# Kernel optimization log

Measured on AMD Instinct MI355X. Metric: run time of the kernel, lower is better.

## Reference

```python
import jax, jax.numpy as jnp
import numpy as np

LMAX, MMAX = 4, 2
L1 = LMAX + 1                      # 5 coefficients with m=0
NL = [LMAX + 1 - m for m in range(MMAX + 1)]   # [5,4,3] degrees per |m|
K = (LMAX + 1) ** 2                # 25 full SH coefficients
KR = NL[0] + 2 * sum(NL[1:])       # 19 coefficients with |m|<=mmax
# degree l of each row in the reduced (m-primary) layout:
# m=0: l=0..4 | m=+1: l=1..4 | m=-1: l=1..4 | m=+2: l=2..4 | m=-2: l=2..4
L_IDX = np.array([0,1,2,3,4, 1,2,3,4, 1,2,3,4, 2,3,4, 2,3,4])


def so2_conv(x, rad, w0, b0, wr1, wi1, wr2, wi2, c_out, extra):
    """SO(2)-equivariant conv over m-primary layout x: [E, KR, c_in].
    rad: optional per-edge radial weights [E, sum_m nl_m*c_in]."""
    E, _, c_in = x.shape
    # m = 0 block
    x0 = x[:, :L1].reshape(E, L1 * c_in)
    if rad is not None:
        x0 = x0 * rad[:, :L1 * c_in]
    y0 = x0 @ w0 + b0
    out0 = y0[:, :L1 * c_out].reshape(E, L1, c_out)
    gating = y0[:, L1 * c_out:] if extra else None
    outs = [out0]
    off_x, off_r = L1, L1 * c_in
    for nl, wr, wi in ((NL[1], wr1, wi1), (NL[2], wr2, wi2)):
        xr = x[:, off_x:off_x + nl].reshape(E, nl * c_in)
        xi = x[:, off_x + nl:off_x + 2 * nl].reshape(E, nl * c_in)
        if rad is not None:
            rm = rad[:, off_r:off_r + nl * c_in]
            xr, xi = xr * rm, xi * rm
        yr = xr @ wr - xi @ wi   # complex-style SO2 mixing
        yi = xi @ wr + xr @ wi
        outs += [yr.reshape(E, nl, c_out), yi.reshape(E, nl, c_out)]
        off_x += 2 * nl
        off_r += nl * c_in
    return jnp.concatenate(outs, axis=1), gating


def gate_act(gating, x):
    """GateActivation: silu on l=0 scalars, sigmoid gates per degree l>=1."""
    E, _, H = x.shape
    g = jax.nn.sigmoid(gating).reshape(E, LMAX, H)
    g_ext = jnp.concatenate([jnp.ones((E, 1, H), x.dtype), g], axis=1)
    out = x * g_ext[:, L_IDX]           # l=0 row gated by 1, replaced below
    return out.at[:, 0].set(jax.nn.silu(x[:, 0]))


def setup_inputs() -> dict:
    key = jax.random.key(0)
    ks = jax.random.split(key, 32)
    E, N, C, H, D, RH = 50000, 2500, 64, 64, 128, 64
    c_in1 = 2 * C
    rad_dim = sum(nl * c_in1 for nl in NL)          # 1536
    extra = LMAX * H                                 # 256

    def w(k, shape):
        return jax.random.normal(k, shape, jnp.float32) / np.sqrt(shape[0])

    inp = {
        'node_feats': jax.random.normal(ks[0], (N, K, C), jnp.float32),
        'edge_embeds': jax.random.normal(ks[1], (E, D), jnp.float32),
        'wigner': jax.random.normal(ks[2], (E, KR, K), jnp.float32) / np.sqrt(K),
        'wigner_inv': jax.random.normal(ks[3], (E, K, KR), jnp.float32) / np.sqrt(KR),
        'edge_envelope': jax.random.uniform(ks[4], (E, 1, 1), jnp.float32),
        'rad_w1': w(ks[5], (D, RH)), 'rad_b1': jnp.zeros((RH,), jnp.float32),
        'rad_w2': w(ks[6], (RH, rad_dim)), 'rad_b2': jnp.zeros((rad_dim,), jnp.float32),
        'w1_m0': w(ks[7], (L1 * c_in1, L1 * H + extra)),
        'b1_m0': jnp.zeros((L1 * H + extra,), jnp.float32),
        'w1_r1': w(ks[8], (NL[1] * c_in1, NL[1] * H)),
        'w1_i1': w(ks[9], (NL[1] * c_in1, NL[1] * H)),
        'w1_r2': w(ks[10], (NL[2] * c_in1, NL[2] * H)),
        'w1_i2': w(ks[11], (NL[2] * c_in1, NL[2] * H)),
        'w2_m0': w(ks[12], (L1 * H, L1 * C)),
        'b2_m0': jnp.zeros((L1 * C,), jnp.float32),
        'w2_r1': w(ks[13], (NL[1] * H, NL[1] * C)),
        'w2_i1': w(ks[14], (NL[1] * H, NL[1] * C)),
        'w2_r2': w(ks[15], (NL[2] * H, NL[2] * C)),
        'w2_i2': w(ks[16], (NL[2] * H, NL[2] * C)),
        'senders': jax.random.randint(ks[17], (E,), 0, N, jnp.int32),
        'receivers': jax.random.randint(ks[18], (E,), 0, N, jnp.int32),
    }
    return inp


def reference(node_feats, edge_embeds, wigner, wigner_inv, edge_envelope,
              rad_w1, rad_b1, rad_w2, rad_b2,
              w1_m0, b1_m0, w1_r1, w1_i1, w1_r2, w1_i2,
              w2_m0, b2_m0, w2_r1, w2_i1, w2_r2, w2_i2,
              senders, receivers):
    num_nodes = node_feats.shape[0]
    C = node_feats.shape[2]
    H = w2_m0.shape[0] // L1
    # gather + concat: [E, K, 2C]
    msg = jnp.concatenate((node_feats[senders], node_feats[receivers]), axis=2)
    # rotate to edge frame, truncated to |m|<=mmax: [E, KR, 2C]
    msg = jnp.einsum('erk,ekc->erc', wigner, msg)
    # per-edge radial weights for conv1
    rad = jax.nn.silu(edge_embeds @ rad_w1 + rad_b1) @ rad_w2 + rad_b2
    msg, gating = so2_conv(msg, rad, w1_m0, b1_m0, w1_r1, w1_i1, w1_r2, w1_i2,
                           c_out=H, extra=LMAX * H)
    msg = gate_act(gating, msg)
    msg, _ = so2_conv(msg, None, w2_m0, b2_m0, w2_r1, w2_i1, w2_r2, w2_i2,
                      c_out=C, extra=0)
    msg = msg * edge_envelope
    # rotate back to global frame: [E, K, C]
    msg = jnp.einsum('ekr,erc->ekc', wigner_inv, msg)
    return jax.ops.segment_sum(msg, receivers, num_segments=num_nodes)
```

## Files before the change

kernel.cpp:

```cpp
#include <hip/hip_runtime.h>


typedef __attribute__((ext_vector_type(8))) short bf16x8;
typedef __attribute__((ext_vector_type(4))) float f32x4;

union U8 { uint4 v; unsigned short s[8]; };

__device__ __forceinline__ unsigned short f2b(float f) {
    unsigned u = __float_as_uint(f);
    unsigned r = (u + 0x7FFFu + ((u >> 16) & 1u)) >> 16;
    return (unsigned short)r;
}
__device__ __forceinline__ float b2f(unsigned short h) {
    return __uint_as_float(((unsigned)h) << 16);
}
__device__ __forceinline__ float sigm_(float x){ return 1.0f/(1.0f+__expf(-x)); }
__device__ __forceinline__ float silu_(float x){ return x/(1.0f+__expf(-x)); }

__device__ __forceinline__ void async16(short* lds, const short* g) {
    __builtin_amdgcn_global_load_lds(
        (const __attribute__((address_space(1))) void*)g,
        (__attribute__((address_space(3))) void*)lds, 16, 0, 0);
}

#define OFF_W1T   0L
#define OFF_W1C1  409600L
#define OFF_W1C2  933888L
#define OFF_V0T   1327104L
#define OFF_V1C   1449984L
#define OFF_V2C   1712128L
#define OFF_RW2T  1908736L
#define W_TOTAL   2007040L
#define NNODES    2500
#define NFT_ELEMS (2500L * 2048L)

__global__ void k_prep(const float* __restrict__ w1m0, const float* __restrict__ w1r1,
                       const float* __restrict__ w1i1, const float* __restrict__ w1r2,
                       const float* __restrict__ w1i2, const float* __restrict__ w2m0,
                       const float* __restrict__ w2r1, const float* __restrict__ w2i1,
                       const float* __restrict__ w2r2, const float* __restrict__ w2i2,
                       const float* __restrict__ rw2, short* __restrict__ W)
{
    long i = (long)blockIdx.x * blockDim.x + threadIdx.x;
    if (i >= W_TOTAL) return;
    float v;
    if (i < OFF_W1C1) {
        int n = (int)(i / 640), k = (int)(i % 640);
        v = (n < 576) ? w1m0[k * 576 + n] : 0.f;
    } else if (i < OFF_W1C2) {
        long j = i - OFF_W1C1; int n = (int)(j >> 10), k = (int)(j & 1023);
        v = (n < 256) ? ((k < 512) ? w1r1[k*256 + n] : -w1i1[(k-512)*256 + n])
                      : ((k < 512) ? w1i1[k*256 + (n-256)] : w1r1[(k-512)*256 + (n-256)]);
    } else if (i < OFF_V0T) {
        long j = i - OFF_W1C2; int n = (int)(j / 768), k = (int)(j % 768);
        v = (n >= 384) ? 0.f
          : (n < 192) ? ((k < 384) ? w1r2[k*192 + n] : -w1i2[(k-384)*192 + n])
                      : ((k < 384) ? w1i2[k*192 + (n-192)] : w1r2[(k-384)*192 + (n-192)]);
    } else if (i < OFF_V1C) {
        long j = i - OFF_V0T; int n = (int)(j / 320), k = (int)(j % 320);
        v = (n < 320) ? w2m0[k * 320 + n] : 0.f;
    } else if (i < OFF_V2C) {
        long j = i - OFF_V1C; int n = (int)(j >> 9), k = (int)(j & 511);
        v = (n < 256) ? ((k < 256) ? w2r1[k*256 + n] : -w2i1[(k-256)*256 + n])
                      : ((k < 256) ? w2i1[k*256 + (n-256)] : w2r1[(k-256)*256 + (n-256)]);
    } else if (i < OFF_RW2T) {
        long j = i - OFF_V2C; int n = (int)(j / 384), k = (int)(j % 384);
        v = (n >= 384) ? 0.f
          : (n < 192) ? ((k < 192) ? w2r2[k*192 + n] : -w2i2[(k-192)*192 + n])
                      : ((k < 192) ? w2i2[k*192 + (n-192)] : w2r2[(k-192)*192 + (n-192)]);
    } else {
        long j = i - OFF_RW2T; int n = (int)(j >> 6), d = (int)(j & 63);
        v = rw2[d * 1536 + n];
    }
    W[i] = (short)f2b(v);
}

__global__ __launch_bounds__(256)
void k_nft(const float* __restrict__ nf, short* __restrict__ nfT)
{
    __shared__ float s_nf[25 * 65];
    const int t = threadIdx.x;
    const long nn = blockIdx.x;
    for (int p = t; p < 1600; p += 256) {
        int r = p >> 6, c = p & 63;
        s_nf[r * 65 + c] = nf[nn * 1600 + p];
    }
    __syncthreads();
    for (int i = t; i < 2048; i += 256) {
        int c = i >> 5, k = i & 31;
        float v = (k < 25) ? s_nf[k * 65 + c] : 0.f;
        nfT[nn * 2048 + i] = (short)f2b(v);
    }
}

__global__ void k_hist(const int* __restrict__ rcv, int* __restrict__ cnt, long e0, long n)
{
    long e = (long)blockIdx.x * 256 + threadIdx.x;
    if (e < n) atomicAdd(&cnt[rcv[e0 + e]], 1);
}

__global__ __launch_bounds__(256)
void k_scan(const int* __restrict__ cnt, int* __restrict__ off, int* __restrict__ nxt)
{
    __shared__ int part[256];
    const int t = threadIdx.x;
    const int base = t * 10;
    int loc[10]; int s = 0;
    #pragma unroll
    for (int j = 0; j < 10; ++j) {
        int idx = base + j;
        int v = (idx < NNODES) ? cnt[idx] : 0;
        loc[j] = s; s += v;
    }
    part[t] = s;
    __syncthreads();
    for (int d = 1; d < 256; d <<= 1) {
        int v = part[t];
        int u = (t >= d) ? part[t - d] : 0;
        __syncthreads();
        part[t] = v + u;
        __syncthreads();
    }
    int excl = (t == 0) ? 0 : part[t - 1];
    #pragma unroll
    for (int j = 0; j < 10; ++j) {
        int idx = base + j;
        if (idx < NNODES) { int o = excl + loc[j]; off[idx] = o; nxt[idx] = o; }
    }
}

__global__ void k_scat(const int* __restrict__ rcv, int* __restrict__ nxt,
                       int* __restrict__ perm, long e0, long n)
{
    long e = (long)blockIdx.x * 256 + threadIdx.x;
    if (e < n) {
        int p = atomicAdd(&nxt[rcv[e0 + e]], 1);
        perm[p] = (int)e;
    }
}

__global__ __launch_bounds__(512)
void k_rad(const float* __restrict__ ee, const float* __restrict__ rw1,
           const float* __restrict__ rb1, const float* __restrict__ rb2,
           const short* __restrict__ RW2T, short* __restrict__ rad,
           long e0, long Etot)
{
    __shared__ __align__(16) short s_h[32 * 64];
    const int t = threadIdx.x, w = t >> 6, l = t & 63, l15 = l & 15, lhi = l >> 4;
    const long eb = (long)blockIdx.x * 32;

    #pragma unroll
    for (int j = 0; j < 4; ++j) {
        int i = t + j * 512;
        int e = i >> 6, d = i & 63;
        long ge = e0 + eb + e;
        float a = rb1[d];
        if (ge < Etot) {
            const float* ep = ee + ge * 128;
            #pragma unroll 16
            for (int dd = 0; dd < 128; ++dd) a = fmaf(ep[dd], rw1[dd * 64 + d], a);
            a = silu_(a);
        } else a = 0.f;
        *(short*)((char*)s_h + e * 128 + ((d * 2) ^ ((e & 7) << 4))) = (short)f2b(a);
    }
    __syncthreads();

    f32x4 acc[6][2][2];
    #pragma unroll
    for (int g = 0; g < 6; ++g)
        #pragma unroll
        for (int mt = 0; mt < 2; ++mt)
            #pragma unroll
            for (int nt = 0; nt < 2; ++nt)
                acc[g][mt][nt] = (f32x4){0.f, 0.f, 0.f, 0.f};

    #pragma unroll
    for (int ks = 0; ks < 2; ++ks) {
        bf16x8 af[2];
        #pragma unroll
        for (int mt = 0; mt < 2; ++mt)
            af[mt] = *(const bf16x8*)((const char*)s_h + (mt * 16 + l15) * 128 +
                                      (((ks << 6) + (lhi << 4)) ^ ((l & 7) << 4)));
        #pragma unroll
        for (int g = 0; g < 6; ++g) {
            int grp = w + g * 8;
            #pragma unroll
            for (int nt = 0; nt < 2; ++nt) {
                int col = grp * 32 + nt * 16 + l15;
                bf16x8 bf = *(const bf16x8*)(RW2T + (long)col * 64 + (ks << 5) + (lhi << 3));
                #pragma unroll
                for (int mt = 0; mt < 2; ++mt)
                    acc[g][mt][nt] = __builtin_amdgcn_mfma_f32_16x16x32_bf16(af[mt], bf, acc[g][mt][nt], 0, 0, 0);
            }
        }
    }
    #pragma unroll
    for (int g = 0; g < 6; ++g)
        #pragma unroll
        for (int nt = 0; nt < 2; ++nt) {
            int col = (w + g * 8) * 32 + nt * 16 + l15;
            float bias = rb2[col];
            #pragma unroll
            for (int mt = 0; mt < 2; ++mt)
                #pragma unroll
                for (int r = 0; r < 4; ++r) {
                    int e = mt * 16 + lhi * 4 + r;
                    rad[(eb + e) * 1536 + col] = (short)f2b(acc[g][mt][nt][r] + bias);
                }
        }
}

__global__ __launch_bounds__(256)
void k_rot2(const float* __restrict__ wig, const short* __restrict__ nfT,
            const short* __restrict__ rad,
            const int* __restrict__ snd, const int* __restrict__ rcv,
            short* __restrict__ X, long e0, long nchunk)
{
    __shared__ float s_wg[4][480];
    __shared__ __align__(16) short s_rot[4][20 * 128];
    const int t = threadIdx.x, w = t >> 6, l = t & 63, l15 = l & 15, lhi = l >> 4;
    const long eb = (long)blockIdx.x * 4;
    const long el = eb + w;
    const bool valid = (el < nchunk);

    for (int p = t; p < 4 * 475; p += 256) {
        int e = p / 475, q = p - e * 475;
        if (eb + e < nchunk) s_wg[e][q] = wig[(e0 + eb + e) * 475 + q];
    }
    __syncthreads();

    if (valid) {
        long ge = e0 + el;
        int n0 = snd[ge], n1 = rcv[ge];
        U8 a0u, a1u;
        #pragma unroll
        for (int j = 0; j < 8; ++j) {
            int k = lhi * 8 + j;
            a0u.s[j] = (k < 25) ? f2b(s_wg[w][l15 * 25 + k]) : (unsigned short)0;
            a1u.s[j] = (l15 < 3 && k < 25) ? f2b(s_wg[w][(16 + l15) * 25 + k]) : (unsigned short)0;
        }
        bf16x8 a0 = *(bf16x8*)&a0u, a1 = *(bf16x8*)&a1u;

        f32x4 acc0[8], acc1[8];
        #pragma unroll
        for (int nt = 0; nt < 8; ++nt) {
            acc0[nt] = (f32x4){0.f, 0.f, 0.f, 0.f};
            acc1[nt] = (f32x4){0.f, 0.f, 0.f, 0.f};
        }
        #pragma unroll
        for (int nt = 0; nt < 8; ++nt) {
            int col = nt * 16 + l15;
            bf16x8 b = *(const bf16x8*)(nfT + (long)(col < 64 ? n0 : n1) * 2048 +
                                        (long)(col & 63) * 32 + (lhi << 3));
            acc0[nt] = __builtin_amdgcn_mfma_f32_16x16x32_bf16(a0, b, acc0[nt], 0, 0, 0);
            acc1[nt] = __builtin_amdgcn_mfma_f32_16x16x32_bf16(a1, b, acc1[nt], 0, 0, 0);
        }
        char* base = (char*)s_rot[w];
        #pragma unroll
        for (int nt = 0; nt < 8; ++nt) {
            int col2 = (nt * 16 + l15) * 2;
            #pragma unroll
            for (int r = 0; r < 4; ++r) {
                int row = lhi * 4 + r;
                *(short*)(base + ((row * 256 + col2) ^ ((row & 7) << 4))) = (short)f2b(acc0[nt][r]);
            }
            if (lhi == 0) {
                #pragma unroll
                for (int r = 0; r < 4; ++r) {
                    int row = 16 + r;
                    *(short*)(base + ((row * 256 + col2) ^ ((row & 7) << 4))) = (short)f2b(acc1[nt][r]);
                }
            }
        }
    }
    __syncthreads();

    short* xp = X + el * 2432;
    if (valid) {
        const short* rp = rad + el * 1536;
        #pragma unroll
        for (int it = 0; it < 5; ++it) {
            int q = l + it * 64;
            if (q < 304) {
                int r = q >> 4, c0 = (q & 15) << 3;
                int rr = (r < 9) ? r : ((r < 16) ? r - 4 : r - 7);
                U8 rot; rot.v = *(uint4*)((char*)s_rot[w] + ((r * 256 + c0 * 2) ^ ((r & 7) << 4)));
                U8 rd;  rd.v  = *(const uint4*)(rp + rr * 128 + c0);
                U8 o;
                #pragma unroll
                for (int j = 0; j < 8; ++j) o.s[j] = f2b(b2f(rot.s[j]) * b2f(rd.s[j]));
                *(uint4*)(xp + q * 8) = o.v;
            }
        }
    } else {
        #pragma unroll
        for (int it = 0; it < 5; ++it) {
            int q = l + it * 64;
            if (q < 304) *(uint4*)(xp + q * 8) = (uint4){0, 0, 0, 0};
        }
    }
}

__global__ __launch_bounds__(256)
void k_gate(short* __restrict__ Zr, long nitems)
{
    long idx = (long)blockIdx.x * 256 + threadIdx.x;
    if (idx >= nitems) return;
    long e = idx / 152;
    int jg = (int)(idx - e * 152);
    int j = jg * 8;
    short* rp = Zr + e * 1536;
    U8 z; z.v = *(const uint4*)(rp + j);
    U8 o;
    if (j < 320) {
        int rr = j >> 6;
        if (rr == 0) {
            #pragma unroll
            for (int q = 0; q < 8; ++q) o.s[q] = f2b(silu_(b2f(z.s[q])));
        } else {
            U8 g; g.v = *(const uint4*)(rp + 1216 + (rr - 1) * 64 + (j & 63));
            #pragma unroll
            for (int q = 0; q < 8; ++q) o.s[q] = f2b(b2f(z.s[q]) * b2f(g.s[q]));
        }
    } else if (j < 832) {
        U8 g; g.v = *(const uint4*)(rp + 1216 + ((j - 320) & 255));
        #pragma unroll
        for (int q = 0; q < 8; ++q) o.s[q] = f2b(b2f(z.s[q]) * b2f(g.s[q]));
    } else {
        int gi = j - 832; if (gi >= 192) gi -= 192;
        U8 g; g.v = *(const uint4*)(rp + 1280 + gi);
        #pragma unroll
        for (int q = 0; q < 8; ++q) o.s[q] = f2b(b2f(z.s[q]) * b2f(g.s[q]));
    }
    *(uint4*)(rp + j) = o.v;
}

template<int Km, int Nreal, int EPI>
__device__ __forceinline__ void gemm_body(
    const short* __restrict__ A, const long RS,
    const short* __restrict__ W, const float* __restrict__ bias,
    short* __restrict__ O, const long OS, const int oofs,
    short* __restrict__ sA, short* __restrict__ sB, const int et, const int cb)
{
    const int t = threadIdx.x, w = t >> 6, l = t & 63, l15 = l & 15, lhi = l >> 4;
    const long eb = (long)et * 128;
    const short* Ap = A + eb * RS;
    const short* Wp = W + (long)cb * Km;

    f32x4 acc[4][4];
    #pragma unroll
    for (int mt = 0; mt < 4; ++mt)
        #pragma unroll
        for (int nt = 0; nt < 4; ++nt)
            acc[mt][nt] = (f32x4){0.f, 0.f, 0.f, 0.f};

    int rowi[4], k8i[4];
    #pragma unroll
    for (int i = 0; i < 4; ++i) {
        int p = t + i * 256, frag = p >> 6, lif = p & 63;
        rowi[i] = ((frag >> 1) << 4) + (lif & 15);
        k8i[i]  = ((frag & 1) << 2) + (lif >> 4);
    }
    const int wb = (t >> 6) << 6;

    constexpr int NCH = Km / 64;
    for (int ch = 0; ch < NCH; ++ch) {
        __syncthreads();
        const int kc = ch * 64;
        #pragma unroll
        for (int i = 0; i < 4; ++i) {
            async16(sA + (wb + i * 256) * 8, Ap + (long)rowi[i] * RS + kc + k8i[i] * 8);
            async16(sB + (wb + i * 256) * 8, Wp + (long)rowi[i] * Km + kc + k8i[i] * 8);
        }
        __syncthreads();
        #pragma unroll
        for (int ks = 0; ks < 2; ++ks) {
            bf16x8 af[4], bf[4];
            #pragma unroll
            for (int mt = 0; mt < 4; ++mt)
                af[mt] = *(const bf16x8*)(sA + ((((w & 1) * 4 + mt) * 2 + ks) * 64 + l) * 8);
            #pragma unroll
            for (int nt = 0; nt < 4; ++nt)
                bf[nt] = *(const bf16x8*)(sB + ((((w >> 1) * 4 + nt) * 2 + ks) * 64 + l) * 8);
            #pragma unroll
            for (int mt = 0; mt < 4; ++mt)
                #pragma unroll
                for (int nt = 0; nt < 4; ++nt)
                    acc[mt][nt] = __builtin_amdgcn_mfma_f32_16x16x32_bf16(af[mt], bf[nt], acc[mt][nt], 0, 0, 0);
        }
    }

    const int r0 = (w & 1) * 64, c0 = (w >> 1) * 64;
    #pragma unroll
    for (int nt = 0; nt < 4; ++nt) {
        int jj = cb + c0 + nt * 16 + l15;
        if (jj < Nreal) {
            float b = (EPI >= 1) ? bias[jj] : 0.f;
            #pragma unroll
            for (int mt = 0; mt < 4; ++mt)
                #pragma unroll
                for (int r = 0; r < 4; ++r) {
                    long e = eb + r0 + mt * 16 + lhi * 4 + r;
                    float v = acc[mt][nt][r] + b;
                    if constexpr (EPI == 2) {
                        if (jj < 320) O[e * OS + jj] = (short)f2b(v);
                        else          O[e * OS + 1216 + (jj - 320)] = (short)f2b(sigm_(v));
                    } else {
                        O[e * OS + oofs + jj] = (short)f2b(v);
                    }
                }
        }
    }
}

__global__ __launch_bounds__(256)
void k_conv1(const short* __restrict__ X, const short* __restrict__ W0,
             const short* __restrict__ W1, const short* __restrict__ W2,
             const float* __restrict__ b1m0, short* __restrict__ Zr, int nbt)
{
    __shared__ __align__(16) short sA[8192];
    __shared__ __align__(16) short sB[8192];
    const int bid = blockIdx.x;
    const int s = bid >> 3;
    const int et = (bid & 7) + ((s / 13) << 3);
    const int ph = s % 13;
    if (et >= nbt) return;
    if (ph < 5)
        gemm_body< 640, 576, 2>(X,        2432, W0, b1m0,   Zr, 1536, 0,   sA, sB, et, ph << 7);
    else if (ph < 9)
        gemm_body<1024, 512, 0>(X + 640,  2432, W1, nullptr, Zr, 1536, 320, sA, sB, et, (ph - 5) << 7);
    else
        gemm_body< 768, 384, 0>(X + 1664, 2432, W2, nullptr, Zr, 1536, 832, sA, sB, et, (ph - 9) << 7);
}

__global__ __launch_bounds__(256)
void k_conv2(const short* __restrict__ Zr, const short* __restrict__ V0,
             const short* __restrict__ V1, const short* __restrict__ V2,
             const float* __restrict__ b2m0, short* __restrict__ Y2, int nbt)
{
    __shared__ __align__(16) short sA[8192];
    __shared__ __align__(16) short sB[8192];
    const int bid = blockIdx.x;
    const int s = bid >> 3;
    const int et = (bid & 7) + ((s / 11) << 3);
    const int ph = s % 11;
    if (et >= nbt) return;
    if (ph < 3)
        gemm_body<320, 320, 1>(Zr,       1536, V0, b2m0,   Y2, 1216, 0,   sA, sB, et, ph << 7);
    else if (ph < 7)
        gemm_body<512, 512, 0>(Zr + 320, 1536, V1, nullptr, Y2, 1216, 320, sA, sB, et, (ph - 3) << 7);
    else
        gemm_body<384, 384, 0>(Zr + 832, 1536, V2, nullptr, Y2, 1216, 832, sA, sB, et, (ph - 7) << 7);
}

__global__ __launch_bounds__(256)
void k_invn(const short* __restrict__ Y2, const float* __restrict__ winv,
            const float* __restrict__ env, const int* __restrict__ cnt,
            const int* __restrict__ off, const int* __restrict__ perm,
            float* __restrict__ out, long e0)
{
    __shared__ __align__(16) short s_y[2][1216];
    __shared__ float s_wv[2][476];
    const int t = threadIdx.x;
    const int n = blockIdx.x;
    const int deg = cnt[n], start = off[n];

    float acc[7];
    #pragma unroll
    for (int j = 0; j < 7; ++j) acc[j] = 0.f;

    auto stage = [&](int i, int b) {
        int el = perm[start + i];
        long ge = e0 + el;
        if (t < 152) ((uint4*)s_y[b])[t] = *(const uint4*)(Y2 + (long)el * 1216 + t * 8);
        for (int p = t; p < 475; p += 256) s_wv[b][p] = winv[ge * 475 + p];
        if (t == 0) s_wv[b][475] = env[ge];
    };

    if (deg > 0) stage(0, 0);
    for (int i = 0; i < deg; ++i) {
        __syncthreads();
        if (i + 1 < deg) stage(i + 1, (i + 1) & 1);
        const short* sy = s_y[i & 1];
        const float* sw = s_wv[i & 1];
        float ev = sw[475];
        #pragma unroll
        for (int j = 0; j < 7; ++j) {
            int f = t + j * 256;
            if (f < 1600) {
                int r = f >> 6, c = f & 63;
                float a = 0.f;
                #pragma unroll
                for (int k = 0; k < 19; ++k)
                    a = fmaf(sw[r * 19 + k], b2f((unsigned short)sy[k * 64 + c]), a);
                acc[j] = fmaf(a, ev, acc[j]);
            }
        }
    }
    #pragma unroll
    for (int j = 0; j < 7; ++j) {
        int f = t + j * 256;
        if (f < 1600) out[(long)n * 1600 + f] += acc[j];
    }
}

extern "C" void kernel_launch(void* const* d_in, const int* in_sizes, int n_in,
                              void* d_out, int out_size, void* d_ws, size_t ws_size,
                              hipStream_t stream)
{
    const float* nf   = (const float*)d_in[0];
    const float* ee   = (const float*)d_in[1];
    const float* wig  = (const float*)d_in[2];
    const float* winv = (const float*)d_in[3];
    const float* env  = (const float*)d_in[4];
    const float* rw1  = (const float*)d_in[5];
    const float* rb1  = (const float*)d_in[6];
    const float* rw2  = (const float*)d_in[7];
    const float* rb2  = (const float*)d_in[8];
    const float* w1m0 = (const float*)d_in[9];
    const float* b1m0 = (const float*)d_in[10];
    const float* w1r1 = (const float*)d_in[11];
    const float* w1i1 = (const float*)d_in[12];
    const float* w1r2 = (const float*)d_in[13];
    const float* w1i2 = (const float*)d_in[14];
    const float* w2m0 = (const float*)d_in[15];
    const float* b2m0 = (const float*)d_in[16];
    const float* w2r1 = (const float*)d_in[17];
    const float* w2i1 = (const float*)d_in[18];
    const float* w2r2 = (const float*)d_in[19];
    const float* w2i2 = (const float*)d_in[20];
    const int*   snd  = (const int*)d_in[21];
    const int*   rcv  = (const int*)d_in[22];
    float* out = (float*)d_out;

    const long E = in_sizes[21];

    short* Wb  = (short*)d_ws;
    short* nfT = Wb + W_TOTAL;
    int* cnt   = (int*)(nfT + NFT_ELEMS);
    int* off   = cnt + 2512;
    int* nxt   = off + 2512;
    int* perm  = nxt + 2512;

    const size_t fixed = (size_t)W_TOTAL * 2 + (size_t)NFT_ELEMS * 2 + 3 * 2512 * 4;
    long cap = (ws_size > fixed) ? (long)((ws_size - fixed) / 7940) : 128;
    long chunk = (cap / 128) * 128;
    if (chunk < 128) chunk = 128;
    long Epad = ((E + 127) / 128) * 128;
    if (chunk > Epad) chunk = Epad;

    short* Xc = (short*)(perm + chunk);
    short* Rc = Xc + chunk * 2432;

    hipMemsetAsync(d_out, 0, (size_t)out_size * sizeof(float), stream);
    k_prep<<<(int)((W_TOTAL + 511) / 512), 512, 0, stream>>>(
        w1m0, w1r1, w1i1, w1r2, w1i2, w2m0, w2r1, w2i1, w2r2, w2i2, rw2, Wb);
    k_nft<<<NNODES, 256, 0, stream>>>(nf, nfT);

    for (long base = 0; base < E; base += chunk) {
        long n = E - base; if (n > chunk) n = chunk;
        int nb2 = (int)((n + 127) / 128);
        int nb8 = ((nb2 + 7) / 8) * 8;
        int nbe = (int)((n + 255) / 256);

        hipMemsetAsync(cnt, 0, NNODES * sizeof(int), stream);
        k_hist<<<nbe, 256, 0, stream>>>(rcv, cnt, base, n);
        k_scan<<<1, 256, 0, stream>>>(cnt, off, nxt);
        k_scat<<<nbe, 256, 0, stream>>>(rcv, nxt, perm, base, n);

        k_rad <<<(int)((n + 31) / 32), 512, 0, stream>>>(ee, rw1, rb1, rb2, Wb + OFF_RW2T, Rc, base, E);
        k_rot2<<<nb2 * 32, 256, 0, stream>>>(wig, nfT, Rc, snd, rcv, Xc, base, n);

        k_conv1<<<nb8 * 13, 256, 0, stream>>>(Xc, Wb + OFF_W1T, Wb + OFF_W1C1, Wb + OFF_W1C2, b1m0, Rc, nb2);

        long nitems = (long)nb2 * 128 * 152;
        k_gate<<<(int)((nitems + 255) / 256), 256, 0, stream>>>(Rc, nitems);

        k_conv2<<<nb8 * 11, 256, 0, stream>>>(Rc, Wb + OFF_V0T, Wb + OFF_V1C, Wb + OFF_V2C, b2m0, Xc, nb2);

        k_invn<<<NNODES, 256, 0, stream>>>(Xc, winv, env, cnt, off, perm, out, base);
    }
    (void)n_in;
}
```

Before: 1.176 ms.

## Replace LDS-staged block GEMM with per-wave direct-global-load MFMA GEMM

The conv GEMMs drop shared-memory staging and block-wide barriers. Each 64-thread block (one wave) now loads its A and B MFMA fragments straight from global memory into registers and computes a 64x64 tile, so four times as many blocks are launched. This removes the __syncthreads cost and LDS traffic. In exchange, the four waves that covered one 128x128 tile no longer share staged data, so more global or L2 traffic goes to uncoalesced 16-byte fragment loads, with less latency hiding than the async LDS path.

```diff
diff --git a/kernel.cpp b/kernel.cpp
--- a/kernel.cpp
+++ b/kernel.cpp
@@ -16,12 +16,6 @@
 }
 __device__ __forceinline__ float sigm_(float x){ return 1.0f/(1.0f+__expf(-x)); }
 __device__ __forceinline__ float silu_(float x){ return x/(1.0f+__expf(-x)); }
-
-__device__ __forceinline__ void async16(short* lds, const short* g) {
-    __builtin_amdgcn_global_load_lds(
-        (const __attribute__((address_space(1))) void*)g,
-        (__attribute__((address_space(3))) void*)lds, 16, 0, 0);
-}
 
 #define OFF_W1T   0L
 #define OFF_W1C1  409600L
@@ -336,16 +330,13 @@
 }
 
 template<int Km, int Nreal, int EPI>
-__device__ __forceinline__ void gemm_body(
+__device__ __forceinline__ void gemm_wave(
     const short* __restrict__ A, const long RS,
     const short* __restrict__ W, const float* __restrict__ bias,
     short* __restrict__ O, const long OS, const int oofs,
-    short* __restrict__ sA, short* __restrict__ sB, const int et, const int cb)
-{
-    const int t = threadIdx.x, w = t >> 6, l = t & 63, l15 = l & 15, lhi = l >> 4;
-    const long eb = (long)et * 128;
-    const short* Ap = A + eb * RS;
-    const short* Wp = W + (long)cb * Km;
+    const long rb, const int cbase)
+{
+    const int l = threadIdx.x & 63, l15 = l & 15, lhi = l >> 4;
 
     f32x4 acc[4][4];
     #pragma unroll
@@ -354,34 +345,30 @@
         for (int nt = 0; nt < 4; ++nt)
             acc[mt][nt] = (f32x4){0.f, 0.f, 0.f, 0.f};
 
-    int rowi[4], k8i[4];
-    #pragma unroll
-    for (int i = 0; i < 4; ++i) {
-        int p = t + i * 256, frag = p >> 6, lif = p & 63;
-        rowi[i] = ((frag >> 1) << 4) + (lif & 15);
-        k8i[i]  = ((frag & 1) << 2) + (lif >> 4);
-    }
-    const int wb = (t >> 6) << 6;
+    const short* Ab = A + (rb + l15) * RS + lhi * 8;
+    const short* Wb = W + (long)(cbase + l15) * Km + lhi * 8;
 
     constexpr int NCH = Km / 64;
+    #pragma unroll 2
     for (int ch = 0; ch < NCH; ++ch) {
-        __syncthreads();
         const int kc = ch * 64;
-        #pragma unroll
-        for (int i = 0; i < 4; ++i) {
-            async16(sA + (wb + i * 256) * 8, Ap + (long)rowi[i] * RS + kc + k8i[i] * 8);
-            async16(sB + (wb + i * 256) * 8, Wp + (long)rowi[i] * Km + kc + k8i[i] * 8);
-        }
-        __syncthreads();
+        bf16x8 af[4], bf[4];
+        #pragma unroll
+        for (int mt = 0; mt < 4; ++mt)
+            af[mt] = *(const bf16x8*)(Ab + (long)mt * 16 * RS + kc);
+        #pragma unroll
+        for (int nt = 0; nt < 4; ++nt)
+            bf[nt] = *(const bf16x8*)(Wb + (long)nt * 16 * Km + kc);
         #pragma unroll
         for (int ks = 0; ks < 2; ++ks) {
-            bf16x8 af[4], bf[4];
-            #pragma unroll
-            for (int mt = 0; mt < 4; ++mt)
-                af[mt] = *(const bf16x8*)(sA + ((((w & 1) * 4 + mt) * 2 + ks) * 64 + l) * 8);
-            #pragma unroll
-            for (int nt = 0; nt < 4; ++nt)
-                bf[nt] = *(const bf16x8*)(sB + ((((w >> 1) * 4 + nt) * 2 + ks) * 64 + l) * 8);
+            if (ks == 1) {
+                #pragma unroll
+                for (int mt = 0; mt < 4; ++mt)
+                    af[mt] = *(const bf16x8*)(Ab + (long)mt * 16 * RS + kc + 32);
+                #pragma unroll
+                for (int nt = 0; nt < 4; ++nt)
+                    bf[nt] = *(const bf16x8*)(Wb + (long)nt * 16 * Km + kc + 32);
+            }
             #pragma unroll
             for (int mt = 0; mt < 4; ++mt)
                 #pragma unroll
@@ -390,17 +377,16 @@
         }
     }
 
-    const int r0 = (w & 1) * 64, c0 = (w >> 1) * 64;
     #pragma unroll
     for (int nt = 0; nt < 4; ++nt) {
-        int jj = cb + c0 + nt * 16 + l15;
+        int jj = cbase + nt * 16 + l15;
         if (jj < Nreal) {
             float b = (EPI >= 1) ? bias[jj] : 0.f;
             #pragma unroll
             for (int mt = 0; mt < 4; ++mt)
                 #pragma unroll
                 for (int r = 0; r < 4; ++r) {
-                    long e = eb + r0 + mt * 16 + lhi * 4 + r;
+                    long e = rb + mt * 16 + lhi * 4 + r;
                     float v = acc[mt][nt][r] + b;
                     if constexpr (EPI == 2) {
                         if (jj < 320) O[e * OS + jj] = (short)f2b(v);
@@ -413,44 +399,52 @@
     }
 }
 
-__global__ __launch_bounds__(256)
+__global__ __launch_bounds__(64)
 void k_conv1(const short* __restrict__ X, const short* __restrict__ W0,
              const short* __restrict__ W1, const short* __restrict__ W2,
              const float* __restrict__ b1m0, short* __restrict__ Zr, int nbt)
 {
-    __shared__ __align__(16) short sA[8192];
-    __shared__ __align__(16) short sB[8192];
     const int bid = blockIdx.x;
     const int s = bid >> 3;
-    const int et = (bid & 7) + ((s / 13) << 3);
-    const int ph = s % 13;
+    const int et = (bid & 7) + ((s / 52) << 3);
+    const int u = s % 52;
+    const int ph = u >> 2, wq = u & 3;
     if (et >= nbt) return;
-    if (ph < 5)
-        gemm_body< 640, 576, 2>(X,        2432, W0, b1m0,   Zr, 1536, 0,   sA, sB, et, ph << 7);
-    else if (ph < 9)
-        gemm_body<1024, 512, 0>(X + 640,  2432, W1, nullptr, Zr, 1536, 320, sA, sB, et, (ph - 5) << 7);
-    else
-        gemm_body< 768, 384, 0>(X + 1664, 2432, W2, nullptr, Zr, 1536, 832, sA, sB, et, (ph - 9) << 7);
-}
-
-__global__ __launch_bounds__(256)
+    const long rb = (long)et * 128 + (wq & 1) * 64;
+    if (ph < 5) {
+        const int cbase = (ph << 7) + (wq >> 1) * 64;
+        gemm_wave< 640, 576, 2>(X,        2432, W0, b1m0,   Zr, 1536, 0,   rb, cbase);
+    } else if (ph < 9) {
+        const int cbase = ((ph - 5) << 7) + (wq >> 1) * 64;
+        gemm_wave<1024, 512, 0>(X + 640,  2432, W1, nullptr, Zr, 1536, 320, rb, cbase);
+    } else {
+        const int cbase = ((ph - 9) << 7) + (wq >> 1) * 64;
+        gemm_wave< 768, 384, 0>(X + 1664, 2432, W2, nullptr, Zr, 1536, 832, rb, cbase);
+    }
+}
+
+__global__ __launch_bounds__(64)
 void k_conv2(const short* __restrict__ Zr, const short* __restrict__ V0,
              const short* __restrict__ V1, const short* __restrict__ V2,
              const float* __restrict__ b2m0, short* __restrict__ Y2, int nbt)
 {
-    __shared__ __align__(16) short sA[8192];
-    __shared__ __align__(16) short sB[8192];
     const int bid = blockIdx.x;
     const int s = bid >> 3;
-    const int et = (bid & 7) + ((s / 11) << 3);
-    const int ph = s % 11;
+    const int et = (bid & 7) + ((s / 44) << 3);
+    const int u = s % 44;
+    const int ph = u >> 2, wq = u & 3;
     if (et >= nbt) return;
-    if (ph < 3)
-        gemm_body<320, 320, 1>(Zr,       1536, V0, b2m0,   Y2, 1216, 0,   sA, sB, et, ph << 7);
-    else if (ph < 7)
-        gemm_body<512, 512, 0>(Zr + 320, 1536, V1, nullptr, Y2, 1216, 320, sA, sB, et, (ph - 3) << 7);
-    else
-        gemm_body<384, 384, 0>(Zr + 832, 1536, V2, nullptr, Y2, 1216, 832, sA, sB, et, (ph - 7) << 7);
+    const long rb = (long)et * 128 + (wq & 1) * 64;
+    if (ph < 3) {
+        const int cbase = (ph << 7) + (wq >> 1) * 64;
+        gemm_wave<320, 320, 1>(Zr,       1536, V0, b2m0,   Y2, 1216, 0,   rb, cbase);
+    } else if (ph < 7) {
+        const int cbase = ((ph - 3) << 7) + (wq >> 1) * 64;
+        gemm_wave<512, 512, 0>(Zr + 320, 1536, V1, nullptr, Y2, 1216, 320, rb, cbase);
+    } else {
+        const int cbase = ((ph - 7) << 7) + (wq >> 1) * 64;
+        gemm_wave<384, 384, 0>(Zr + 832, 1536, V2, nullptr, Y2, 1216, 832, rb, cbase);
+    }
 }
 
 __global__ __launch_bounds__(256)
@@ -571,12 +565,12 @@
         k_rad <<<(int)((n + 31) / 32), 512, 0, stream>>>(ee, rw1, rb1, rb2, Wb + OFF_RW2T, Rc, base, E);
         k_rot2<<<nb2 * 32, 256, 0, stream>>>(wig, nfT, Rc, snd, rcv, Xc, base, n);
 
-        k_conv1<<<nb8 * 13, 256, 0, stream>>>(Xc, Wb + OFF_W1T, Wb + OFF_W1C1, Wb + OFF_W1C2, b1m0, Rc, nb2);
+        k_conv1<<<nb8 * 52, 64, 0, stream>>>(Xc, Wb + OFF_W1T, Wb + OFF_W1C1, Wb + OFF_W1C2, b1m0, Rc, nb2);
 
         long nitems = (long)nb2 * 128 * 152;
         k_gate<<<(int)((nitems + 255) / 256), 256, 0, stream>>>(Rc, nitems);
 
-        k_conv2<<<nb8 * 11, 256, 0, stream>>>(Rc, Wb + OFF_V0T, Wb + OFF_V1C, Wb + OFF_V2C, b2m0, Xc, nb2);
+        k_conv2<<<nb8 * 44, 64, 0, stream>>>(Rc, Wb + OFF_V0T, Wb + OFF_V1C, Wb + OFF_V2C, b2m0, Xc, nb2);
 
         k_invn<<<NNODES, 256, 0, stream>>>(Xc, winv, env, cnt, off, perm, out, base);
     }
```

New measurement: 1.406 ms. +19.5%, slower.

## Widen SO2 conv GEMM tiles to 128x256 with 512 threads and XOR-swizzled LDS

Applied to the files above, without the earlier changes.

Each conv1 and conv2 GEMM block now uses 8 waves covering a 128x256 output tile instead of 4 waves on 128x128. This halves the number of times the A (edge-feature) tile is reloaded across N-blocks. The LDS staging moves from a fragment-major layout to row-major with an XOR swizzle on the 16-byte k-chunks to avoid bank conflicts. The trade-off is more padding waste where the output widths (576, 320, 384) do not divide 256, so more MFMA work is thrown away. The wider tiles also read weight rows past the real widths and use more LDS per block, which lowers occupancy.

```diff
diff --git a/kernel.cpp b/kernel.cpp
--- a/kernel.cpp
+++ b/kernel.cpp
@@ -343,6 +343,7 @@
     short* __restrict__ sA, short* __restrict__ sB, const int et, const int cb)
 {
     const int t = threadIdx.x, w = t >> 6, l = t & 63, l15 = l & 15, lhi = l >> 4;
+    const int wm = w & 1, wn = w >> 1;
     const long eb = (long)et * 128;
     const short* Ap = A + eb * RS;
     const short* Wp = W + (long)cb * Km;
@@ -354,34 +355,48 @@
         for (int nt = 0; nt < 4; ++nt)
             acc[mt][nt] = (f32x4){0.f, 0.f, 0.f, 0.f};
 
-    int rowi[4], k8i[4];
+    int rowA[2], k8A[2];
+    #pragma unroll
+    for (int i = 0; i < 2; ++i) {
+        int s = i * 512 + t;
+        rowA[i] = s >> 3;
+        k8A[i]  = (s & 7) ^ (rowA[i] & 7);
+    }
+    int rowB[4], k8B[4];
     #pragma unroll
     for (int i = 0; i < 4; ++i) {
-        int p = t + i * 256, frag = p >> 6, lif = p & 63;
-        rowi[i] = ((frag >> 1) << 4) + (lif & 15);
-        k8i[i]  = ((frag & 1) << 2) + (lif >> 4);
-    }
-    const int wb = (t >> 6) << 6;
-
+        int s = i * 512 + t;
+        rowB[i] = s >> 3;
+        k8B[i]  = (s & 7) ^ (rowB[i] & 7);
+    }
+    const int wb = w << 6;
+
+    const int rx = l & 7;
     constexpr int NCH = Km / 64;
     for (int ch = 0; ch < NCH; ++ch) {
+        const int kc = ch * 64;
         __syncthreads();
-        const int kc = ch * 64;
-        #pragma unroll
-        for (int i = 0; i < 4; ++i) {
-            async16(sA + (wb + i * 256) * 8, Ap + (long)rowi[i] * RS + kc + k8i[i] * 8);
-            async16(sB + (wb + i * 256) * 8, Wp + (long)rowi[i] * Km + kc + k8i[i] * 8);
-        }
+        #pragma unroll
+        for (int i = 0; i < 2; ++i)
+            async16(sA + (i * 512 + wb) * 8, Ap + (long)rowA[i] * RS + kc + k8A[i] * 8);
+        #pragma unroll
+        for (int i = 0; i < 4; ++i)
+            async16(sB + (i * 512 + wb) * 8, Wp + (long)rowB[i] * Km + kc + k8B[i] * 8);
         __syncthreads();
         #pragma unroll
         for (int ks = 0; ks < 2; ++ks) {
+            const int ko = (((ks << 2) + lhi) ^ rx) << 3;
             bf16x8 af[4], bf[4];
             #pragma unroll
-            for (int mt = 0; mt < 4; ++mt)
-                af[mt] = *(const bf16x8*)(sA + ((((w & 1) * 4 + mt) * 2 + ks) * 64 + l) * 8);
-            #pragma unroll
-            for (int nt = 0; nt < 4; ++nt)
-                bf[nt] = *(const bf16x8*)(sB + ((((w >> 1) * 4 + nt) * 2 + ks) * 64 + l) * 8);
+            for (int mt = 0; mt < 4; ++mt) {
+                int row = wm * 64 + mt * 16 + l15;
+                af[mt] = *(const bf16x8*)(sA + row * 64 + ko);
+            }
+            #pragma unroll
+            for (int nt = 0; nt < 4; ++nt) {
+                int row = wn * 64 + nt * 16 + l15;
+                bf[nt] = *(const bf16x8*)(sB + row * 64 + ko);
+            }
             #pragma unroll
             for (int mt = 0; mt < 4; ++mt)
                 #pragma unroll
@@ -390,7 +405,7 @@
         }
     }
 
-    const int r0 = (w & 1) * 64, c0 = (w >> 1) * 64;
+    const int r0 = wm * 64, c0 = wn * 64;
     #pragma unroll
     for (int nt = 0; nt < 4; ++nt) {
         int jj = cb + c0 + nt * 16 + l15;
@@ -413,44 +428,44 @@
     }
 }
 
-__global__ __launch_bounds__(256)
+__global__ __launch_bounds__(512)
 void k_conv1(const short* __restrict__ X, const short* __restrict__ W0,
              const short* __restrict__ W1, const short* __restrict__ W2,
              const float* __restrict__ b1m0, short* __restrict__ Zr, int nbt)
 {
     __shared__ __align__(16) short sA[8192];
-    __shared__ __align__(16) short sB[8192];
+    __shared__ __align__(16) short sB[16384];
     const int bid = blockIdx.x;
     const int s = bid >> 3;
-    const int et = (bid & 7) + ((s / 13) << 3);
-    const int ph = s % 13;
+    const int et = (bid & 7) + ((s / 7) << 3);
+    const int ph = s % 7;
     if (et >= nbt) return;
-    if (ph < 5)
-        gemm_body< 640, 576, 2>(X,        2432, W0, b1m0,   Zr, 1536, 0,   sA, sB, et, ph << 7);
-    else if (ph < 9)
-        gemm_body<1024, 512, 0>(X + 640,  2432, W1, nullptr, Zr, 1536, 320, sA, sB, et, (ph - 5) << 7);
+    if (ph < 3)
+        gemm_body< 640, 576, 2>(X,        2432, W0, b1m0,   Zr, 1536, 0,   sA, sB, et, ph << 8);
+    else if (ph < 5)
+        gemm_body<1024, 512, 0>(X + 640,  2432, W1, nullptr, Zr, 1536, 320, sA, sB, et, (ph - 3) << 8);
     else
-        gemm_body< 768, 384, 0>(X + 1664, 2432, W2, nullptr, Zr, 1536, 832, sA, sB, et, (ph - 9) << 7);
-}
-
-__global__ __launch_bounds__(256)
+        gemm_body< 768, 384, 0>(X + 1664, 2432, W2, nullptr, Zr, 1536, 832, sA, sB, et, (ph - 5) << 8);
+}
+
+__global__ __launch_bounds__(512)
 void k_conv2(const short* __restrict__ Zr, const short* __restrict__ V0,
              const short* __restrict__ V1, const short* __restrict__ V2,
              const float* __restrict__ b2m0, short* __restrict__ Y2, int nbt)
 {
     __shared__ __align__(16) short sA[8192];
-    __shared__ __align__(16) short sB[8192];
+    __shared__ __align__(16) short sB[16384];
     const int bid = blockIdx.x;
     const int s = bid >> 3;
-    const int et = (bid & 7) + ((s / 11) << 3);
-    const int ph = s % 11;
+    const int et = (bid & 7) + ((s / 6) << 3);
+    const int ph = s % 6;
     if (et >= nbt) return;
-    if (ph < 3)
-        gemm_body<320, 320, 1>(Zr,       1536, V0, b2m0,   Y2, 1216, 0,   sA, sB, et, ph << 7);
-    else if (ph < 7)
-        gemm_body<512, 512, 0>(Zr + 320, 1536, V1, nullptr, Y2, 1216, 320, sA, sB, et, (ph - 3) << 7);
+    if (ph < 2)
+        gemm_body<320, 320, 1>(Zr,       1536, V0, b2m0,   Y2, 1216, 0,   sA, sB, et, ph << 8);
+    else if (ph < 4)
+        gemm_body<512, 512, 0>(Zr + 320, 1536, V1, nullptr, Y2, 1216, 320, sA, sB, et, (ph - 2) << 8);
     else
-        gemm_body<384, 384, 0>(Zr + 832, 1536, V2, nullptr, Y2, 1216, 832, sA, sB, et, (ph - 7) << 7);
+        gemm_body<384, 384, 0>(Zr + 832, 1536, V2, nullptr, Y2, 1216, 832, sA, sB, et, (ph - 4) << 8);
 }
 
 __global__ __launch_bounds__(256)
@@ -571,12 +586,12 @@
         k_rad <<<(int)((n + 31) / 32), 512, 0, stream>>>(ee, rw1, rb1, rb2, Wb + OFF_RW2T, Rc, base, E);
         k_rot2<<<nb2 * 32, 256, 0, stream>>>(wig, nfT, Rc, snd, rcv, Xc, base, n);
 
-        k_conv1<<<nb8 * 13, 256, 0, stream>>>(Xc, Wb + OFF_W1T, Wb + OFF_W1C1, Wb + OFF_W1C2, b1m0, Rc, nb2);
+        k_conv1<<<nb8 * 7, 512, 0, stream>>>(Xc, Wb + OFF_W1T, Wb + OFF_W1C1, Wb + OFF_W1C2, b1m0, Rc, nb2);
 
         long nitems = (long)nb2 * 128 * 152;
         k_gate<<<(int)((nitems + 255) / 256), 256, 0, stream>>>(Rc, nitems);
 
-        k_conv2<<<nb8 * 11, 256, 0, stream>>>(Rc, Wb + OFF_V0T, Wb + OFF_V1C, Wb + OFF_V2C, b2m0, Xc, nb2);
+        k_conv2<<<nb8 * 6, 512, 0, stream>>>(Rc, Wb + OFF_V0T, Wb + OFF_V1C, Wb + OFF_V2C, b2m0, Xc, nb2);
 
         k_invn<<<NNODES, 256, 0, stream>>>(Xc, winv, env, cnt, off, perm, out, base);
     }
```

Measured after the change: 1.034 ms. -12.1%, faster.
